# Kernel tuning notes

Measured on AMD Instinct MI355X. Metric: run time of the kernel, lower is better.

The kernel has to match this reference:

```python
import jax, jax.numpy as jnp
import numpy as np

N, D, V = 2048, 64, 2048


def setup_inputs() -> dict:
    key = jax.random.key(0)
    k_ids, k_emb, k_tree, k_map = jax.random.split(key, 4)
    language_ids = jax.random.randint(k_ids, (N,), 0, V)
    language_embeddings = jax.random.normal(k_emb, (N, D), dtype=jnp.float32)
    # symmetric distance tables, mimicking the symmetric try/except dict lookup
    t = jax.random.uniform(k_tree, (V, V), dtype=jnp.float32)
    tree_dist = (t + t.T) * 0.5
    m = jax.random.uniform(k_map, (V, V), dtype=jnp.float32)
    map_dist = (m + m.T) * 0.5
    return {
        "language_ids": language_ids,
        "language_embeddings": language_embeddings,
        "tree_dist": tree_dist,
        "map_dist": map_dist,
    }


def reference(language_ids, language_embeddings, tree_dist, map_dist):
    # pairwise mean-L1 distance between embeddings: [N, N]
    emb_dist = jnp.mean(
        jnp.abs(language_embeddings[:, None, :] - language_embeddings[None, :, :]),
        axis=-1,
    )
    # largest_value_map_dist as computed in __init__
    largest = jnp.max(map_dist)
    ii = language_ids[:, None]  # [N, 1]
    jj = language_ids[None, :]  # [1, N]
    metric = (tree_dist[ii, jj] + map_dist[ii, jj] / largest) * 0.5  # [N, N]
    # pairs with equal language ids are skipped in the original loop
    mask = (ii != jj).astype(emb_dist.dtype)
    per_pair = jnp.abs(emb_dist - metric) * mask
    return jnp.sum(per_pair) / jnp.sum(mask)
```

## Files before the change

kernel.cpp:

```cpp
#include <hip/hip_runtime.h>
#include <hip/hip_bf16.h>

#define NL 2048
#define DE 64
#define VV 2048
#define BI 64
#define BJ 32
#define NTI (NL / BI)
#define NTJ (NL / BJ)
#define NBLK 1056
#define STI 66
#define STJ 36


__global__ __launch_bounds__(1024) void prep_kernel(const int* __restrict__ ids,
                                                    const float4* __restrict__ m4,
                                                    const float4* __restrict__ t4,
                                                    float* __restrict__ pmax,
                                                    int* __restrict__ perm,
                                                    int* __restrict__ sids) {
    const int t = threadIdx.x;
    const int lane = t & 63, wave = t >> 6;
    const int b = blockIdx.x;

    if (b < 256) {
        const float4* p = m4 + (size_t)b * 4096;
        const float4* q = t4 + (size_t)b * 4096;
        const float4 x0 = p[t], x1 = p[t + 1024], x2 = p[t + 2048], x3 = p[t + 3072];
        const float4 y0 = q[t], y1 = q[t + 1024], y2 = q[t + 2048], y3 = q[t + 3072];
        float v = fmaxf(fmaxf(fmaxf(x0.x, x0.y), fmaxf(x0.z, x0.w)),
                        fmaxf(fmaxf(x1.x, x1.y), fmaxf(x1.z, x1.w)));
        v = fmaxf(v, fmaxf(fmaxf(x2.x, x2.y), fmaxf(x2.z, x2.w)));
        v = fmaxf(v, fmaxf(fmaxf(x3.x, x3.y), fmaxf(x3.z, x3.w)));
        const float warm = (y0.x + y0.w) + (y1.y + y1.z) + (y2.x + y2.w) + (y3.y + y3.z);
        v = fmaxf(v, warm - 1e30f);
        #pragma unroll
        for (int o = 32; o > 0; o >>= 1)
            v = fmaxf(v, __shfl_down(v, o));
        __shared__ float wl[16];
        if (lane == 0) wl[wave] = v;
        __syncthreads();
        if (t == 0) {
            float m = wl[0];
            #pragma unroll
            for (int i = 1; i < 16; ++i) m = fmaxf(m, wl[i]);
            pmax[b] = m;
        }
    } else {
        __shared__ unsigned hist[VV];
        __shared__ unsigned offs[VV];
        __shared__ unsigned wtot[16];
        __shared__ unsigned wexc[16];
        hist[2 * t] = 0u; hist[2 * t + 1] = 0u;
        __syncthreads();
        const int id0 = ids[2 * t], id1 = ids[2 * t + 1];
        atomicAdd(&hist[id0], 1u);
        atomicAdd(&hist[id1], 1u);
        __syncthreads();
        const unsigned h0 = hist[2 * t], h1 = hist[2 * t + 1];
        const unsigned s = h0 + h1;
        unsigned ps = s;
        #pragma unroll
        for (int o = 1; o < 64; o <<= 1) {
            unsigned u = __shfl_up(ps, o);
            if (lane >= o) ps += u;
        }
        if (lane == 63) wtot[wave] = ps;
        __syncthreads();
        if (wave == 0 && lane < 16) {
            unsigned v = wtot[lane];
            unsigned pv = v;
            #pragma unroll
            for (int o = 1; o < 16; o <<= 1) {
                unsigned u = __shfl_up(pv, o);
                if (lane >= o) pv += u;
            }
            wexc[lane] = pv - v;
        }
        __syncthreads();
        const unsigned ex = wexc[wave] + ps - s;
        offs[2 * t]     = ex;
        offs[2 * t + 1] = ex + h0;
        __syncthreads();
        unsigned p0 = atomicAdd(&offs[id0], 1u);
        perm[p0] = 2 * t;     sids[p0] = id0;
        unsigned p1 = atomicAdd(&offs[id1], 1u);
        perm[p1] = 2 * t + 1; sids[p1] = id1;
    }
}

__global__ __launch_bounds__(512, 8) void loss_kernel(
    const float* __restrict__ emb,
    const float* __restrict__ tree, const float* __restrict__ mapd,
    const int* __restrict__ perm, const int* __restrict__ sids,
    const float* __restrict__ pmax,
    float* __restrict__ psum, unsigned* __restrict__ pcnt)
{
    const int t = threadIdx.x;

    const int orig = blockIdx.x;
    const int L = (orig & 7) * (NBLK / 8) + (orig >> 3);

    int bi = (int)((65.0f - sqrtf(4225.0f - 4.0f * (float)L)) * 0.5f);
    if (bi > NTI - 1) bi = NTI - 1;
    if (bi < 0) bi = 0;
    while (65 * bi - bi * bi > L) --bi;
    while (65 * (bi + 1) - (bi + 1) * (bi + 1) <= L) ++bi;
    const int bj = 2 * bi + (L - (65 * bi - bi * bi));

    const int i0 = (t >> 4) * 2;
    const int j0 = (t & 15) * 2;

    int ia[2], ja[2];
    ia[0] = sids[bi * BI + i0];     ia[1] = sids[bi * BI + i0 + 1];
    ja[0] = sids[bj * BJ + j0];     ja[1] = sids[bj * BJ + j0 + 1];
    float tg[2][2], mg[2][2];
    #pragma unroll
    for (int s = 0; s < 2; ++s)
        #pragma unroll
        for (int c = 0; c < 2; ++c) {
            const int off = ia[s] * VV + ja[c];
            tg[s][c] = tree[off];
            mg[s][c] = mapd[off];
        }

    __shared__ __align__(16) float Eit[DE][STI];
    __shared__ __align__(16) float Ejt[DE][STJ];
    __shared__ float wm[8];

    float pv = pmax[t & 255];

    {
        const int r  = t & 63;
        const int c0 = (t >> 6) << 3;
        const int gi = perm[bi * BI + r];
        const float4* pa = (const float4*)(emb + (size_t)gi * DE + c0);
        float4 a0 = pa[0], a1 = pa[1];
        Eit[c0 + 0][r] = a0.x; Eit[c0 + 1][r] = a0.y; Eit[c0 + 2][r] = a0.z; Eit[c0 + 3][r] = a0.w;
        Eit[c0 + 4][r] = a1.x; Eit[c0 + 5][r] = a1.y; Eit[c0 + 6][r] = a1.z; Eit[c0 + 7][r] = a1.w;

        const int rj  = t & 31;
        const int cj0 = (t >> 5) << 2;
        const int gj = perm[bj * BJ + rj];
        const float4* pb = (const float4*)(emb + (size_t)gj * DE + cj0);
        float4 b0 = pb[0];
        Ejt[cj0 + 0][rj] = b0.x; Ejt[cj0 + 1][rj] = b0.y; Ejt[cj0 + 2][rj] = b0.z; Ejt[cj0 + 3][rj] = b0.w;
    }
    #pragma unroll
    for (int o = 32; o > 0; o >>= 1)
        pv = fmaxf(pv, __shfl_down(pv, o));
    if ((t & 63) == 0) wm[t >> 6] = pv;
    __syncthreads();

    float bm = fmaxf(fmaxf(wm[0], wm[1]), fmaxf(wm[2], wm[3]));
    bm = fmaxf(bm, fmaxf(fmaxf(wm[4], wm[5]), fmaxf(wm[6], wm[7])));
    const float inv = 1.0f / bm;

    float acc[2][2];
    acc[0][0] = 0.0f; acc[0][1] = 0.0f; acc[1][0] = 0.0f; acc[1][1] = 0.0f;

    #pragma unroll 2
    for (int k = 0; k < 16; ++k) {
        #pragma unroll
        for (int q = 0; q < 4; ++q) {
            const int d = 4 * k + q;
            const float2 a = *(const float2*)&Eit[d][i0];
            const float2 b = *(const float2*)&Ejt[d][j0];
            acc[0][0] += fabsf(a.x - b.x); acc[0][1] += fabsf(a.x - b.y);
            acc[1][0] += fabsf(a.y - b.x); acc[1][1] += fabsf(a.y - b.y);
        }
    }

    float pp = 0.0f;
    unsigned cnt = 0;
    #pragma unroll
    for (int s = 0; s < 2; ++s) {
        const int posi = bi * BI + i0 + s;
        #pragma unroll
        for (int c = 0; c < 2; ++c) {
            const int posj = bj * BJ + j0 + c;
            if (posi < posj && ia[s] != ja[c]) {
                const float metric = (tg[s][c] + mg[s][c] * inv) * 0.5f;
                pp += 2.0f * fabsf(acc[s][c] * (1.0f / (float)DE) - metric);
                cnt += 2u;
            }
        }
    }

    #pragma unroll
    for (int o = 32; o > 0; o >>= 1) {
        pp  += __shfl_down(pp, o);
        cnt += __shfl_down(cnt, o);
    }
    __shared__ float    wsum_l[8];
    __shared__ unsigned wcnt_l[8];
    if ((t & 63) == 0) { wsum_l[t >> 6] = pp; wcnt_l[t >> 6] = cnt; }
    __syncthreads();
    if (t == 0) {
        float    S = 0.0f;
        unsigned C = 0u;
        #pragma unroll
        for (int w = 0; w < 8; ++w) { S += wsum_l[w]; C += wcnt_l[w]; }
        psum[L] = S;
        pcnt[L] = C;
    }
}

__global__ __launch_bounds__(1024) void finalize_kernel(const float* __restrict__ psum,
                                                        const unsigned* __restrict__ pcnt,
                                                        float* __restrict__ out) {
    const int t = threadIdx.x;
    const int lane = t & 63, wave = t >> 6;
    double s = 0.0;
    unsigned c = 0;
    for (int i = t; i < NBLK; i += 1024) { s += (double)psum[i]; c += pcnt[i]; }
    #pragma unroll
    for (int o = 32; o > 0; o >>= 1) {
        s += __shfl_down(s, o);
        c += __shfl_down(c, o);
    }
    __shared__ double   sl[16];
    __shared__ unsigned cl[16];
    if (lane == 0) { sl[wave] = s; cl[wave] = c; }
    __syncthreads();
    if (t == 0) {
        double   S = sl[0];
        unsigned C = cl[0];
        #pragma unroll
        for (int i = 1; i < 16; ++i) { S += sl[i]; C += cl[i]; }
        out[0] = (float)(S / (double)C);
    }
}

extern "C" void kernel_launch(void* const* d_in, const int* in_sizes, int n_in,
                              void* d_out, int out_size, void* d_ws, size_t ws_size,
                              hipStream_t stream) {
    const int*   ids  = (const int*)d_in[0];
    const float* emb  = (const float*)d_in[1];
    const float* tree = (const float*)d_in[2];
    const float* mapd = (const float*)d_in[3];
    float* out = (float*)d_out;

    float*    pmax = (float*)d_ws;
    int*      perm = (int*)((char*)d_ws + 1024);
    int*      sids = (int*)((char*)d_ws + 9216);
    float*    psum = (float*)((char*)d_ws + 17408);
    unsigned* pcnt = (unsigned*)((char*)d_ws + 21632);

    prep_kernel<<<257, 1024, 0, stream>>>(ids, (const float4*)mapd, (const float4*)tree,
                                          pmax, perm, sids);

    loss_kernel<<<NBLK, 512, 0, stream>>>(emb, tree, mapd, perm, sids, pmax, psum, pcnt);

    finalize_kernel<<<1, 1024, 0, stream>>>(psum, pcnt, out);
}
```

Measured before the change: 101.4 us.

## Pre-permute embeddings into sorted order in prep kernel and drop block swizzle

The prep kernel's sort block now gathers embedding rows into a sorted contiguous buffer. The loss kernel can then load its row tiles directly, with no indirect lookup through perm. The blockIdx swizzle in the loss kernel is also removed, and the sort block moves to block 0 so it starts early. The single sort block now does a serial 512 KB gather, which could lengthen the prep kernel's critical path.

New measurement: 110.5 us. +9.0%, slower.

```diff
diff --git a/kernel.cpp b/kernel.cpp
--- a/kernel.cpp
+++ b/kernel.cpp
@@ -16,16 +16,19 @@
 __global__ __launch_bounds__(1024) void prep_kernel(const int* __restrict__ ids,
                                                     const float4* __restrict__ m4,
                                                     const float4* __restrict__ t4,
+                                                    const float4* __restrict__ e4,
                                                     float* __restrict__ pmax,
                                                     int* __restrict__ perm,
-                                                    int* __restrict__ sids) {
+                                                    int* __restrict__ sids,
+                                                    float4* __restrict__ embS4) {
     const int t = threadIdx.x;
     const int lane = t & 63, wave = t >> 6;
     const int b = blockIdx.x;
 
-    if (b < 256) {
-        const float4* p = m4 + (size_t)b * 4096;
-        const float4* q = t4 + (size_t)b * 4096;
+    if (b > 0) {
+        const int sl = b - 1;
+        const float4* p = m4 + (size_t)sl * 4096;
+        const float4* q = t4 + (size_t)sl * 4096;
         const float4 x0 = p[t], x1 = p[t + 1024], x2 = p[t + 2048], x3 = p[t + 3072];
         const float4 y0 = q[t], y1 = q[t + 1024], y2 = q[t + 2048], y3 = q[t + 3072];
         float v = fmaxf(fmaxf(fmaxf(x0.x, x0.y), fmaxf(x0.z, x0.w)),
@@ -44,11 +47,12 @@
             float m = wl[0];
             #pragma unroll
             for (int i = 1; i < 16; ++i) m = fmaxf(m, wl[i]);
-            pmax[b] = m;
+            pmax[sl] = m;
         }
     } else {
         __shared__ unsigned hist[VV];
         __shared__ unsigned offs[VV];
+        __shared__ int      lp[NL];
         __shared__ unsigned wtot[16];
         __shared__ unsigned wexc[16];
         hist[2 * t] = 0u; hist[2 * t + 1] = 0u;
@@ -83,24 +87,27 @@
         offs[2 * t + 1] = ex + h0;
         __syncthreads();
         unsigned p0 = atomicAdd(&offs[id0], 1u);
-        perm[p0] = 2 * t;     sids[p0] = id0;
+        perm[p0] = 2 * t;     sids[p0] = id0;     lp[p0] = 2 * t;
         unsigned p1 = atomicAdd(&offs[id1], 1u);
-        perm[p1] = 2 * t + 1; sids[p1] = id1;
+        perm[p1] = 2 * t + 1; sids[p1] = id1;     lp[p1] = 2 * t + 1;
+        __syncthreads();
+        for (int v = t; v < NL * (DE / 4); v += 1024) {
+            const int row = v >> 4;
+            embS4[v] = e4[lp[row] * (DE / 4) + (v & 15)];
+        }
     }
 }
 
 __global__ __launch_bounds__(512, 8) void loss_kernel(
-    const float* __restrict__ emb,
+    const float* __restrict__ embS,
     const float* __restrict__ tree, const float* __restrict__ mapd,
-    const int* __restrict__ perm, const int* __restrict__ sids,
+    const int* __restrict__ sids,
     const float* __restrict__ pmax,
     float* __restrict__ psum, unsigned* __restrict__ pcnt)
 {
     const int t = threadIdx.x;
 
-    const int orig = blockIdx.x;
-    const int L = (orig & 7) * (NBLK / 8) + (orig >> 3);
-
+    const int L = blockIdx.x;
     int bi = (int)((65.0f - sqrtf(4225.0f - 4.0f * (float)L)) * 0.5f);
     if (bi > NTI - 1) bi = NTI - 1;
     if (bi < 0) bi = 0;
@@ -133,16 +140,14 @@
     {
         const int r  = t & 63;
         const int c0 = (t >> 6) << 3;
-        const int gi = perm[bi * BI + r];
-        const float4* pa = (const float4*)(emb + (size_t)gi * DE + c0);
+        const float4* pa = (const float4*)(embS + (size_t)(bi * BI + r) * DE + c0);
         float4 a0 = pa[0], a1 = pa[1];
         Eit[c0 + 0][r] = a0.x; Eit[c0 + 1][r] = a0.y; Eit[c0 + 2][r] = a0.z; Eit[c0 + 3][r] = a0.w;
         Eit[c0 + 4][r] = a1.x; Eit[c0 + 5][r] = a1.y; Eit[c0 + 6][r] = a1.z; Eit[c0 + 7][r] = a1.w;
 
         const int rj  = t & 31;
         const int cj0 = (t >> 5) << 2;
-        const int gj = perm[bj * BJ + rj];
-        const float4* pb = (const float4*)(emb + (size_t)gj * DE + cj0);
+        const float4* pb = (const float4*)(embS + (size_t)(bj * BJ + rj) * DE + cj0);
         float4 b0 = pb[0];
         Ejt[cj0 + 0][rj] = b0.x; Ejt[cj0 + 1][rj] = b0.y; Ejt[cj0 + 2][rj] = b0.z; Ejt[cj0 + 3][rj] = b0.w;
     }
@@ -246,11 +251,13 @@
     int*      sids = (int*)((char*)d_ws + 9216);
     float*    psum = (float*)((char*)d_ws + 17408);
     unsigned* pcnt = (unsigned*)((char*)d_ws + 21632);
+    float*    embS = (float*)((char*)d_ws + 32768);
 
     prep_kernel<<<257, 1024, 0, stream>>>(ids, (const float4*)mapd, (const float4*)tree,
-                                          pmax, perm, sids);
-
-    loss_kernel<<<NBLK, 512, 0, stream>>>(emb, tree, mapd, perm, sids, pmax, psum, pcnt);
+                                          (const float4*)emb, pmax, perm, sids,
+                                          (float4*)embS);
+
+    loss_kernel<<<NBLK, 512, 0, stream>>>(embS, tree, mapd, sids, pmax, psum, pcnt);
 
     finalize_kernel<<<1, 1024, 0, stream>>>(psum, pcnt, out);
 }
```
